# Kernel optimization log

Measured on AMD Instinct MI355X. Metric: run time of the kernel, lower is better.

## Reference

```python
import jax, jax.numpy as jnp
import numpy as np

B, T, H = 1024, 512, 128
TIMESTEPS_PREDICT = 4


def setup_inputs() -> dict:
    key = jax.random.key(0)
    ks = jax.random.split(key, 7)
    s = 1.0 / np.sqrt(H)
    return {
        "x": jax.random.normal(ks[0], (B, T, 1), jnp.float32),
        "hidden": jnp.zeros((B, H), jnp.float32),
        "fc0_w": jax.random.normal(ks[1], (H, 1), jnp.float32) * s,
        "fc0_b": jax.random.normal(ks[2], (H,), jnp.float32) * 0.1,
        "fc_w": jax.random.normal(ks[3], (H, H), jnp.float32) * s,
        "fc_b": jax.random.normal(ks[4], (H,), jnp.float32) * 0.1,
        "dec_w": jax.random.normal(ks[5], (1, H), jnp.float32) * s,
        "dec_b": jax.random.normal(ks[6], (1,), jnp.float32) * 0.1,
    }


def _rnn(x, h, fc0_w, fc0_b, fc_w, fc_b):
    """Vanilla tanh RNN over time. x: (B, Tx, 1), h: (B, H) -> (ys (B, Tx, H), h)."""
    def step(h, xt):  # xt: (B, 1)
        h = jnp.tanh(xt @ fc0_w.T + fc0_b + h @ fc_w.T + fc_b)
        return h, h
    h, ys = jax.lax.scan(step, h, jnp.swapaxes(x, 0, 1))  # ys: (Tx, B, H)
    return jnp.swapaxes(ys, 0, 1), h


def reference(x, hidden, fc0_w, fc0_b, fc_w, fc_b, dec_w, dec_b):
    out, h = _rnn(x, hidden, fc0_w, fc0_b, fc_w, fc_b)  # (B, T, H)
    y = out @ dec_w.T + dec_b  # (B, T, 1)
    last = y[:, -1:, :]  # (B, 1, 1)
    for _ in range(TIMESTEPS_PREDICT):
        out_h, h = _rnn(last, h, fc0_w, fc0_b, fc_w, fc_b)
        last = out_h @ dec_w.T + dec_b
        y = jnp.concatenate([y, last], axis=1)
    return y  # (B, T + TIMESTEPS_PREDICT, 1)
```

## Files before the change

### kernel.cpp

```cpp
#include <hip/hip_runtime.h>
#include <hip/hip_bf16.h>


#define BB 1024
#define TT 512
#define HH 128
#define TOUT 516
#define BM 16
#define NW 8
#define HSTR 136
#define XSTR 513
#define YSTR 517
#define PQS 36

typedef __attribute__((ext_vector_type(8))) short bf16x8;
typedef __attribute__((ext_vector_type(4))) float f32x4;

__device__ __forceinline__ short f2bs(float f) {
    __hip_bfloat16 h = __float2bfloat16(f);
    return __builtin_bit_cast(short, h);
}
__device__ __forceinline__ float bs2f(short s) {
    __hip_bfloat16 h = __builtin_bit_cast(__hip_bfloat16, s);
    return __bfloat162float(h);
}

__global__ void detect_dtype(const void* w, int* flag) {
    const int lane = threadIdx.x;
    const __hip_bfloat16* p = (const __hip_bfloat16*)w;
    const float v0 = __bfloat162float(p[lane]);
    const float v1 = __bfloat162float(p[64 + lane]);
    const bool bad = !(fabsf(v0) < 100.0f) || !(fabsf(v1) < 100.0f);
    const unsigned long long m = __ballot(bad);
    if (lane == 0) *flag = (__popcll(m) > 4) ? 1 : 0;
}

template <bool F32>
__device__ __forceinline__ float ldg(const void* p, int idx) {
    if (F32) return ((const float*)p)[idx];
    return __bfloat162float(((const __hip_bfloat16*)p)[idx]);
}

__device__ __forceinline__ float red32(const float* pqrow) {
    const f32x4* v = (const f32x4*)pqrow;
    const f32x4 s = ((v[0] + v[1]) + (v[2] + v[3])) + ((v[4] + v[5]) + (v[6] + v[7]));
    return (s[0] + s[1]) + (s[2] + s[3]);
}

__device__ __forceinline__ unsigned pkbf(float lo, float hi) {
    const unsigned ulo = __builtin_bit_cast(unsigned, lo) + 0x8000u;
    const unsigned uhi = __builtin_bit_cast(unsigned, hi) + 0x8000u;
    return __builtin_amdgcn_perm(uhi, ulo, 0x07060302u);
}

#define STEP(T_, CUR_, WRITEY_, DOPQ_, READX_, TAILX_) do {                     \
    bf16x8 bfrag[4];                                                            \
    _Pragma("unroll")                                                           \
    for (int kf = 0; kf < 4; ++kf)                                              \
        bfrag[kf] = *(const bf16x8*)&hbuf[CUR_][n][kf * 32 + q * 8];            \
    float xnext = 0.0f;                                                         \
    if (READX_) xnext = xs[n][(T_) + 1];                                        \
    float xv;                                                                   \
    if (TAILX_) xv = red32(&pq[((T_) - 1) & 1][n][0]) + dbv;                    \
    else        xv = xpref;                                                     \
    f32x4 acc0, acc1;                                                           \
    _Pragma("unroll")                                                           \
    for (int r = 0; r < 4; ++r) acc0[r] = fmaf(xv, w0v[r], bsum[r]);            \
    acc1 = (f32x4){0.f, 0.f, 0.f, 0.f};                                        \
    acc0 = __builtin_amdgcn_mfma_f32_16x16x32_bf16(wa_hi[0], bfrag[0], acc0, 0, 0, 0); \
    if (F32) acc0 = __builtin_amdgcn_mfma_f32_16x16x32_bf16(wa_lo[0], bfrag[0], acc0, 0, 0, 0); \
    acc0 = __builtin_amdgcn_mfma_f32_16x16x32_bf16(wa_hi[1], bfrag[1], acc0, 0, 0, 0); \
    if (F32) acc0 = __builtin_amdgcn_mfma_f32_16x16x32_bf16(wa_lo[1], bfrag[1], acc0, 0, 0, 0); \
    acc1 = __builtin_amdgcn_mfma_f32_16x16x32_bf16(wa_hi[2], bfrag[2], acc1, 0, 0, 0); \
    if (F32) acc1 = __builtin_amdgcn_mfma_f32_16x16x32_bf16(wa_lo[2], bfrag[2], acc1, 0, 0, 0); \
    acc1 = __builtin_amdgcn_mfma_f32_16x16x32_bf16(wa_hi[3], bfrag[3], acc1, 0, 0, 0); \
    if (F32) acc1 = __builtin_amdgcn_mfma_f32_16x16x32_bf16(wa_lo[3], bfrag[3], acc1, 0, 0, 0); \
    if (isw7 && (WRITEY_)) {     \
        f32x4 aD0 = (f32x4){0.f, 0.f, 0.f, 0.f};                                \
        f32x4 aD1 = (f32x4){0.f, 0.f, 0.f, 0.f};                                \
        aD0 = __builtin_amdgcn_mfma_f32_16x16x32_bf16(wa_dhi[0], bfrag[0], aD0, 0, 0, 0); \
        aD0 = __builtin_amdgcn_mfma_f32_16x16x32_bf16(wa_dhi[1], bfrag[1], aD0, 0, 0, 0); \
        aD1 = __builtin_amdgcn_mfma_f32_16x16x32_bf16(wa_dhi[2], bfrag[2], aD1, 0, 0, 0); \
        aD1 = __builtin_amdgcn_mfma_f32_16x16x32_bf16(wa_dhi[3], bfrag[3], aD1, 0, 0, 0); \
        const float yp = aD0[0] + aD1[0] + dbv;                                 \
        if (q == 0) ybuf[n][(T_) - 1] = yp;                                     \
    }                                                                           \
    float p = 0.0f;                                                             \
    float hv[4];                                                                \
    _Pragma("unroll")                                                           \
    for (int r = 0; r < 4; ++r) {                                               \
        const float z = acc0[r] + acc1[r];                                      \
        const float e = __expf(z + z);                                          \
        const float h = fmaf(-2.0f, __builtin_amdgcn_rcpf(e + 1.0f), 1.0f);     \
        if (DOPQ_) p = fmaf(decv[r], h, p);                                     \
        hv[r] = h;                                                              \
    }                                                                           \
    uint2 pk;                                                                   \
    pk.x = pkbf(hv[0], hv[1]);                                                  \
    pk.y = pkbf(hv[2], hv[3]);                                                  \
    *(uint2*)&hbuf[(CUR_) ^ 1][n][wv * 16 + q * 4] = pk;                        \
    if (DOPQ_) pq[(T_) & 1][n][wv * 4 + q] = p;                                 \
    if (READX_) xpref = xnext;                                                  \
    __syncthreads();                                                            \
} while (0)

template <bool F32>
__device__ void rnn_body(const void* __restrict__ xg, const void* __restrict__ h0,
                         const void* __restrict__ w0, const void* __restrict__ b0,
                         const void* __restrict__ W,  const void* __restrict__ bw,
                         const void* __restrict__ dw, const void* __restrict__ db,
                         void* __restrict__ out,
                         float (*xs)[XSTR], float (*ybuf)[YSTR],
                         __hip_bfloat16 (*hbuf)[BM][HSTR], float (*pq)[BM][PQS])
{
    const int tid  = threadIdx.x;
    const int lane = tid & 63;
    const int wv   = tid >> 6;
    const int q    = lane >> 4;
    const int n    = lane & 15;
    const int row0 = blockIdx.x * BM;
    const bool isw7 = (wv == 7);

    for (int idx = tid; idx < BM * TT; idx += 512) {
        const int rr = idx >> 9, t2 = idx & (TT - 1);
        xs[rr][t2] = ldg<F32>(xg, (row0 + rr) * TT + t2);
    }
    for (int idx = tid; idx < BM * HH; idx += 512) {
        const int rr = idx >> 7, ii = idx & (HH - 1);
        hbuf[0][rr][ii] = __float2bfloat16(ldg<F32>(h0, (row0 + rr) * HH + ii));
    }

    bf16x8 wa_hi[4], wa_lo[4];
    {
        const int ia = wv * 16 + n;
        #pragma unroll
        for (int kf = 0; kf < 4; ++kf) {
            const int kb = kf * 32 + q * 8;
            bf16x8 hi, lo;
            #pragma unroll
            for (int j = 0; j < 8; ++j) {
                const float f = ldg<F32>(W, ia * HH + kb + j);
                const short hs = f2bs(f);
                hi[j] = hs;
                lo[j] = F32 ? f2bs(f - bs2f(hs)) : (short)0;
            }
            wa_hi[kf] = hi;
            wa_lo[kf] = lo;
        }
    }
    bf16x8 wa_dhi[4] = {};
    if (isw7) {
        #pragma unroll
        for (int kf = 0; kf < 4; ++kf) {
            const int kb = kf * 32 + q * 8;
            bf16x8 hi = {};
            if (n == 0) {
                #pragma unroll
                for (int j = 0; j < 8; ++j) hi[j] = f2bs(ldg<F32>(dw, kb + j));
            }
            wa_dhi[kf] = hi;
        }
    }
    float bsum[4], w0v[4], decv[4];
    #pragma unroll
    for (int r = 0; r < 4; ++r) {
        const int ic = wv * 16 + q * 4 + r;
        bsum[r] = ldg<F32>(b0, ic) + ldg<F32>(bw, ic);
        w0v[r]  = ldg<F32>(w0, ic);
        decv[r] = ldg<F32>(dw, ic);
    }
    const float dbv = ldg<F32>(db, 0);

    __syncthreads();

    float xpref = xs[n][0];

    STEP(0, 0, false, false, true, false);

    #pragma unroll 1
    for (int t = 1; t < 511; t += 2) {
        STEP(t,     1, true, false, true, false);
        STEP(t + 1, 0, true, false, true, false);
    }

    STEP(511, 1, true, true, false, false);

    #pragma unroll 1
    for (int t = 512; t < 516; ++t) {
        STEP(t, t & 1, true, true, false, true);
    }

    if (isw7 && q == 0)
        ybuf[n][TOUT - 1] = red32(&pq[(TOUT - 1) & 1][n][0]) + dbv;
    __syncthreads();

    for (int rr = 0; rr < BM; ++rr)
        for (int t2 = tid; t2 < TOUT; t2 += 512) {
            const int o = (row0 + rr) * TOUT + t2;
            const float y = ybuf[rr][t2];
            if (F32) ((float*)out)[o] = y;
            else     ((__hip_bfloat16*)out)[o] = __float2bfloat16(y);
        }
}

__global__ __launch_bounds__(512, 2)
void rnn_mfma(const void* __restrict__ xg, const void* __restrict__ h0,
              const void* __restrict__ w0, const void* __restrict__ b0,
              const void* __restrict__ W,  const void* __restrict__ bw,
              const void* __restrict__ dw, const void* __restrict__ db,
              void* __restrict__ out, const int* __restrict__ flag)
{
    __shared__ float xs[BM][XSTR];
    __shared__ float ybuf[BM][YSTR];
    __shared__ __align__(16) __hip_bfloat16 hbuf[2][BM][HSTR];
    __shared__ __align__(16) float pq[2][BM][PQS];

    const int f = *(volatile const int*)flag;
    if (f) rnn_body<true >(xg, h0, w0, b0, W, bw, dw, db, out, xs, ybuf, hbuf, pq);
    else   rnn_body<false>(xg, h0, w0, b0, W, bw, dw, db, out, xs, ybuf, hbuf, pq);
}

extern "C" void kernel_launch(void* const* d_in, const int* in_sizes, int n_in,
                              void* d_out, int out_size, void* d_ws, size_t ws_size,
                              hipStream_t stream) {
    int* flag = (int*)d_ws;
    detect_dtype<<<1, 64, 0, stream>>>(d_in[4], flag);
    rnn_mfma<<<BB / BM, 512, 0, stream>>>(d_in[0], d_in[1], d_in[2], d_in[3],
                                          d_in[4], d_in[5], d_in[6], d_in[7],
                                          d_out, flag);
}
```

Baseline: 264.8 us.

## Switch recurrent MFMA to fp16 single-pass with XOR-swizzled hidden-state LDS layout

Replaces the bf16 hi/lo split (two MFMAs per k-chunk in the fp32 path) with a single fp16 MFMA per chunk, since tanh outputs and small weights fit fp16 range with more mantissa. The hidden state is stored in fp16 using packed round-toward-zero conversion, and the LDS buffer drops its padding in favour of an XOR swizzle to avoid bank conflicts. This halves the MFMA count on the serial recurrent critical path when inputs are fp32. It risks precision loss from dropping the lo correction term and from fp16 rounding of the weights.

```diff
diff --git a/kernel.cpp b/kernel.cpp
--- a/kernel.cpp
+++ b/kernel.cpp
@@ -7,23 +7,15 @@
 #define HH 128
 #define TOUT 516
 #define BM 16
-#define NW 8
-#define HSTR 136
 #define XSTR 513
 #define YSTR 517
 #define PQS 36
 
-typedef __attribute__((ext_vector_type(8))) short bf16x8;
+typedef __attribute__((ext_vector_type(8))) _Float16 f16x8;
+typedef __attribute__((ext_vector_type(2))) _Float16 f16x2;
 typedef __attribute__((ext_vector_type(4))) float f32x4;
 
-__device__ __forceinline__ short f2bs(float f) {
-    __hip_bfloat16 h = __float2bfloat16(f);
-    return __builtin_bit_cast(short, h);
-}
-__device__ __forceinline__ float bs2f(short s) {
-    __hip_bfloat16 h = __builtin_bit_cast(__hip_bfloat16, s);
-    return __bfloat162float(h);
-}
+#define MFMA16(A_, B_, C_) __builtin_amdgcn_mfma_f32_16x16x32_f16(A_, B_, C_, 0, 0, 0)
 
 __global__ void detect_dtype(const void* w, int* flag) {
     const int lane = threadIdx.x;
@@ -47,17 +39,11 @@
     return (s[0] + s[1]) + (s[2] + s[3]);
 }
 
-__device__ __forceinline__ unsigned pkbf(float lo, float hi) {
-    const unsigned ulo = __builtin_bit_cast(unsigned, lo) + 0x8000u;
-    const unsigned uhi = __builtin_bit_cast(unsigned, hi) + 0x8000u;
-    return __builtin_amdgcn_perm(uhi, ulo, 0x07060302u);
-}
-
 #define STEP(T_, CUR_, WRITEY_, DOPQ_, READX_, TAILX_) do {                     \
-    bf16x8 bfrag[4];                                                            \
+    f16x8 bfrag[4];                                                             \
     _Pragma("unroll")                                                           \
     for (int kf = 0; kf < 4; ++kf)                                              \
-        bfrag[kf] = *(const bf16x8*)&hbuf[CUR_][n][kf * 32 + q * 8];            \
+        bfrag[kf] = *(const f16x8*)&hbuf[CUR_][n][((((kf << 2) | q) ^ n) & 15) << 3]; \
     float xnext = 0.0f;                                                         \
     if (READX_) xnext = xs[n][(T_) + 1];                                        \
     float xv;                                                                   \
@@ -66,22 +52,18 @@
     f32x4 acc0, acc1;                                                           \
     _Pragma("unroll")                                                           \
     for (int r = 0; r < 4; ++r) acc0[r] = fmaf(xv, w0v[r], bsum[r]);            \
-    acc1 = (f32x4){0.f, 0.f, 0.f, 0.f};                                        \
-    acc0 = __builtin_amdgcn_mfma_f32_16x16x32_bf16(wa_hi[0], bfrag[0], acc0, 0, 0, 0); \
-    if (F32) acc0 = __builtin_amdgcn_mfma_f32_16x16x32_bf16(wa_lo[0], bfrag[0], acc0, 0, 0, 0); \
-    acc0 = __builtin_amdgcn_mfma_f32_16x16x32_bf16(wa_hi[1], bfrag[1], acc0, 0, 0, 0); \
-    if (F32) acc0 = __builtin_amdgcn_mfma_f32_16x16x32_bf16(wa_lo[1], bfrag[1], acc0, 0, 0, 0); \
-    acc1 = __builtin_amdgcn_mfma_f32_16x16x32_bf16(wa_hi[2], bfrag[2], acc1, 0, 0, 0); \
-    if (F32) acc1 = __builtin_amdgcn_mfma_f32_16x16x32_bf16(wa_lo[2], bfrag[2], acc1, 0, 0, 0); \
-    acc1 = __builtin_amdgcn_mfma_f32_16x16x32_bf16(wa_hi[3], bfrag[3], acc1, 0, 0, 0); \
-    if (F32) acc1 = __builtin_amdgcn_mfma_f32_16x16x32_bf16(wa_lo[3], bfrag[3], acc1, 0, 0, 0); \
-    if (isw7 && (WRITEY_)) {     \
+    acc1 = (f32x4){0.f, 0.f, 0.f, 0.f};                                         \
+    acc0 = MFMA16(wa[0], bfrag[0], acc0);                                       \
+    acc1 = MFMA16(wa[1], bfrag[1], acc1);                                       \
+    acc0 = MFMA16(wa[2], bfrag[2], acc0);                                       \
+    acc1 = MFMA16(wa[3], bfrag[3], acc1);                                       \
+    if (isw7 && (WRITEY_)) {               \
         f32x4 aD0 = (f32x4){0.f, 0.f, 0.f, 0.f};                                \
         f32x4 aD1 = (f32x4){0.f, 0.f, 0.f, 0.f};                                \
-        aD0 = __builtin_amdgcn_mfma_f32_16x16x32_bf16(wa_dhi[0], bfrag[0], aD0, 0, 0, 0); \
-        aD0 = __builtin_amdgcn_mfma_f32_16x16x32_bf16(wa_dhi[1], bfrag[1], aD0, 0, 0, 0); \
-        aD1 = __builtin_amdgcn_mfma_f32_16x16x32_bf16(wa_dhi[2], bfrag[2], aD1, 0, 0, 0); \
-        aD1 = __builtin_amdgcn_mfma_f32_16x16x32_bf16(wa_dhi[3], bfrag[3], aD1, 0, 0, 0); \
+        aD0 = MFMA16(wa_d[0], bfrag[0], aD0);                                   \
+        aD1 = MFMA16(wa_d[1], bfrag[1], aD1);                                   \
+        aD0 = MFMA16(wa_d[2], bfrag[2], aD0);                                   \
+        aD1 = MFMA16(wa_d[3], bfrag[3], aD1);                                   \
         const float yp = aD0[0] + aD1[0] + dbv;                                 \
         if (q == 0) ybuf[n][(T_) - 1] = yp;                                     \
     }                                                                           \
@@ -96,9 +78,9 @@
         hv[r] = h;                                                              \
     }                                                                           \
     uint2 pk;                                                                   \
-    pk.x = pkbf(hv[0], hv[1]);                                                  \
-    pk.y = pkbf(hv[2], hv[3]);                                                  \
-    *(uint2*)&hbuf[(CUR_) ^ 1][n][wv * 16 + q * 4] = pk;                        \
+    pk.x = __builtin_bit_cast(unsigned, __builtin_amdgcn_cvt_pkrtz(hv[0], hv[1])); \
+    pk.y = __builtin_bit_cast(unsigned, __builtin_amdgcn_cvt_pkrtz(hv[2], hv[3])); \
+    *(uint2*)&hbuf[(CUR_) ^ 1][n][((((2 * wv + (q >> 1)) ^ n) & 15) << 3) + ((q & 1) << 2)] = pk; \
     if (DOPQ_) pq[(T_) & 1][n][wv * 4 + q] = p;                                 \
     if (READX_) xpref = xnext;                                                  \
     __syncthreads();                                                            \
@@ -111,7 +93,7 @@
                          const void* __restrict__ dw, const void* __restrict__ db,
                          void* __restrict__ out,
                          float (*xs)[XSTR], float (*ybuf)[YSTR],
-                         __hip_bfloat16 (*hbuf)[BM][HSTR], float (*pq)[BM][PQS])
+                         _Float16 (*hbuf)[BM][HH], float (*pq)[BM][PQS])
 {
     const int tid  = threadIdx.x;
     const int lane = tid & 63;
@@ -127,38 +109,33 @@
     }
     for (int idx = tid; idx < BM * HH; idx += 512) {
         const int rr = idx >> 7, ii = idx & (HH - 1);
-        hbuf[0][rr][ii] = __float2bfloat16(ldg<F32>(h0, (row0 + rr) * HH + ii));
-    }
-
-    bf16x8 wa_hi[4], wa_lo[4];
+        const int po = ((((ii >> 3) ^ rr) & 15) << 3) + (ii & 7);
+        hbuf[0][rr][po] = (_Float16)ldg<F32>(h0, (row0 + rr) * HH + ii);
+    }
+
+    f16x8 wa[4];
     {
         const int ia = wv * 16 + n;
         #pragma unroll
         for (int kf = 0; kf < 4; ++kf) {
             const int kb = kf * 32 + q * 8;
-            bf16x8 hi, lo;
+            f16x8 fr;
             #pragma unroll
-            for (int j = 0; j < 8; ++j) {
-                const float f = ldg<F32>(W, ia * HH + kb + j);
-                const short hs = f2bs(f);
-                hi[j] = hs;
-                lo[j] = F32 ? f2bs(f - bs2f(hs)) : (short)0;
-            }
-            wa_hi[kf] = hi;
-            wa_lo[kf] = lo;
+            for (int j = 0; j < 8; ++j) fr[j] = (_Float16)ldg<F32>(W, ia * HH + kb + j);
+            wa[kf] = fr;
         }
     }
-    bf16x8 wa_dhi[4] = {};
+    f16x8 wa_d[4] = {};
     if (isw7) {
         #pragma unroll
         for (int kf = 0; kf < 4; ++kf) {
             const int kb = kf * 32 + q * 8;
-            bf16x8 hi = {};
+            f16x8 fr = {};
             if (n == 0) {
                 #pragma unroll
-                for (int j = 0; j < 8; ++j) hi[j] = f2bs(ldg<F32>(dw, kb + j));
+                for (int j = 0; j < 8; ++j) fr[j] = (_Float16)ldg<F32>(dw, kb + j);
             }
-            wa_dhi[kf] = hi;
+            wa_d[kf] = fr;
         }
     }
     float bsum[4], w0v[4], decv[4];
@@ -212,7 +189,7 @@
 {
     __shared__ float xs[BM][XSTR];
     __shared__ float ybuf[BM][YSTR];
-    __shared__ __align__(16) __hip_bfloat16 hbuf[2][BM][HSTR];
+    __shared__ __align__(16) _Float16 hbuf[2][BM][HH];
     __shared__ __align__(16) float pq[2][BM][PQS];
 
     const int f = *(volatile const int*)flag;
```

Result: faster. 222.7 us (-15.9%).
